# Kernel tuning notes

Measured on AMD Instinct MI355X. Metric: run time of the kernel, lower is better.

## Reference

```python
import jax, jax.numpy as jnp
import numpy as np

C = 64
DQ = C // 8  # query/key channel dim


def setup_inputs() -> dict:
    key = jax.random.key(0)
    ks = jax.random.split(key, 8)
    B, H, W = 8, 64, 64
    x = jax.random.normal(ks[0], (B, C, H, W), dtype=jnp.float32)
    # 1x1 conv weights stored as [out, in] matrices (kernel dims squeezed)
    wq = jax.random.normal(ks[1], (DQ, C), dtype=jnp.float32) * 0.05
    bq = jax.random.normal(ks[2], (DQ,), dtype=jnp.float32) * 0.05
    wk = jax.random.normal(ks[3], (DQ, C), dtype=jnp.float32) * 0.05
    bk = jax.random.normal(ks[4], (DQ,), dtype=jnp.float32) * 0.05
    wv = jax.random.normal(ks[5], (C, C), dtype=jnp.float32) * 0.05
    bv = jax.random.normal(ks[6], (C,), dtype=jnp.float32) * 0.05
    gamma = jax.random.normal(ks[7], (1,), dtype=jnp.float32)
    return {"x": x, "wq": wq, "bq": bq, "wk": wk, "bk": bk,
            "wv": wv, "bv": bv, "gamma": gamma}


def reference(x, wq, bq, wk, bk, wv, bv, gamma):
    B, Cc, H, W = x.shape
    N = H * W
    xf = x.reshape(B, Cc, N)                      # [B, C, N]
    # 1x1 convs == channel matmuls
    q = jnp.einsum('dc,bcn->bdn', wq, xf) + bq[None, :, None]   # [B, DQ, N]
    k = jnp.einsum('dc,bcn->bdn', wk, xf) + bk[None, :, None]   # [B, DQ, N]
    v = jnp.einsum('oc,bcn->bon', wv, xf) + bv[None, :, None]   # [B, C, N]
    # energy[b, m, n] = sum_d q[b, d, m] * k[b, d, n]
    energy = jnp.einsum('bdm,bdn->bmn', q, k)                   # [B, N, N]
    attention = jax.nn.softmax(energy, axis=-1)
    # out[b, c, m] = sum_n v[b, c, n] * attention[b, m, n]
    out = jnp.einsum('bcn,bmn->bcm', v, attention).reshape(B, Cc, H, W)
    return gamma[0] * out + x
```

## Files before the change

### kernel.cpp

```cpp
#include <hip/hip_runtime.h>
#include <math.h>

#define NTOK 4096
#define CCH  64
#define LOG2E 1.4426950408889634f
#define NSPLIT 4

typedef __attribute__((ext_vector_type(8)))  short bf16x8;
typedef __attribute__((ext_vector_type(4)))  float f32x4;
typedef __attribute__((ext_vector_type(16))) float f32x16;
typedef __attribute__((ext_vector_type(2)))  unsigned int uint32x2;

__device__ __forceinline__ unsigned short f2bf_rne(float f) {
    unsigned int u = __float_as_uint(f);
    u += 0x7FFFu + ((u >> 16) & 1u);
    return (unsigned short)(u >> 16);
}
__device__ __forceinline__ float bf2f(unsigned short u) {
    return __uint_as_float(((unsigned int)u) << 16);
}

__global__ __launch_bounds__(256) void proj_kernel(
    const float* __restrict__ x,
    const float* __restrict__ wq, const float* __restrict__ bq,
    const float* __restrict__ wk, const float* __restrict__ bk,
    const float* __restrict__ wv, const float* __restrict__ bv,
    unsigned short* __restrict__ qt, unsigned short* __restrict__ kt,
    unsigned short* __restrict__ vbf)
{
    __shared__ unsigned short xsb[64 * 68];
    __shared__ unsigned short wa[80 * 68];
    __shared__ unsigned short vtmp[64 * 66];
    __shared__ float bb[80];

    const int t  = threadIdx.x;
    const int b  = blockIdx.x >> 6;
    const int n0 = (blockIdx.x & 63) << 6;

    const int lane = t & 63;
    const int w    = t >> 6;
    const int l15  = lane & 15;
    const int g    = lane >> 4;

    {
        const int n  = t & 63;
        const int c0 = t >> 6;
        #pragma unroll
        for (int r = 0; r < 16; ++r) {
            const int c = c0 + 4 * r;
            xsb[n * 68 + c] = f2bf_rne(x[((size_t)(b * CCH + c)) * NTOK + n0 + n]);
        }
    }
    #pragma unroll
    for (int r = 0; r < 16; ++r) {
        const int i = t + 256 * r;
        wa[(i >> 6) * 68 + (i & 63)] = f2bf_rne(wv[i]);
    }
    {
        const int i0 = t, i1 = t + 256;
        wa[(64 + (i0 >> 6)) * 68 + (i0 & 63)] = f2bf_rne(wq[i0] * LOG2E);
        wa[(64 + (i1 >> 6)) * 68 + (i1 & 63)] = f2bf_rne(wq[i1] * LOG2E);
        wa[(72 + (i0 >> 6)) * 68 + (i0 & 63)] = f2bf_rne(wk[i0]);
        wa[(72 + (i1 >> 6)) * 68 + (i1 & 63)] = f2bf_rne(wk[i1]);
    }
    if (t < 80) {
        float bias;
        if (t < 64)      bias = bv[t];
        else if (t < 72) bias = bq[t - 64] * LOG2E;
        else             bias = bk[t - 72];
        bb[t] = bias;
    }
    __syncthreads();

    f32x4 acc[5];
    #pragma unroll
    for (int mt = 0; mt < 5; ++mt) acc[mt] = (f32x4){0.f, 0.f, 0.f, 0.f};
    #pragma unroll
    for (int kc = 0; kc < 2; ++kc) {
        const bf16x8 bx = *(const bf16x8*)&xsb[(w * 16 + l15) * 68 + kc * 32 + g * 8];
        #pragma unroll
        for (int mt = 0; mt < 5; ++mt) {
            const bf16x8 aw = *(const bf16x8*)&wa[(mt * 16 + l15) * 68 + kc * 32 + g * 8];
            acc[mt] = __builtin_amdgcn_mfma_f32_16x16x32_bf16(aw, bx, acc[mt], 0, 0, 0);
        }
    }

    const int n = w * 16 + l15;
    #pragma unroll
    for (int mt = 0; mt < 4; ++mt) {
        #pragma unroll
        for (int r = 0; r < 4; ++r) {
            const int c = mt * 16 + g * 4 + r;
            vtmp[c * 66 + 4 * l15 + w] = f2bf_rne(acc[mt][r] + bb[c]);
        }
    }
    {
        unsigned short vals[4];
        #pragma unroll
        for (int r = 0; r < 4; ++r)
            vals[r] = f2bf_rne(acc[4][r] + bb[64 + g * 4 + r]);
        const unsigned int lo = (unsigned int)vals[0] | ((unsigned int)vals[1] << 16);
        const unsigned int hi = (unsigned int)vals[2] | ((unsigned int)vals[3] << 16);
        unsigned short* dst = ((g < 2) ? qt : kt) +
                              ((size_t)(b * NTOK + n0 + n)) * 8 + (g & 1) * 4;
        *(uint32x2*)dst = (uint32x2){lo, hi};
    }
    __syncthreads();

    {
        const int c = t >> 2;
        const int q = t & 3;
        unsigned short* dst = vbf + ((size_t)(b * CCH + c)) * NTOK + n0 + q * 16;
        *(bf16x8*)dst       = *(const bf16x8*)&vtmp[c * 66 + q * 16];
        *(bf16x8*)(dst + 8) = *(const bf16x8*)&vtmp[c * 66 + q * 16 + 8];
    }
}

__global__ __launch_bounds__(256, 4) void attn_kernel(
    const unsigned short* __restrict__ qt, const unsigned short* __restrict__ kt,
    const unsigned short* __restrict__ vbf,
    unsigned short* __restrict__ opart, float* __restrict__ lpart, int B)
{
    __shared__ unsigned short qs[64 * 32];
    __shared__ unsigned short ks[64 * 40];
    __shared__ unsigned short vs[64 * 88];
    __shared__ unsigned short ps[64 * 88];

    const int t    = threadIdx.x;
    const int lane = t & 63;
    const int w    = t >> 6;
    const int p    = blockIdx.x / (B * 64);
    const int rest = blockIdx.x % (B * 64);
    const int b    = rest >> 6;
    const int m0   = (rest & 63) << 6;

    const int l15 = lane & 15;
    const int g   = lane >> 4;
    const int l31 = lane & 31;
    const int h   = lane >> 5;

    if (t < 64) {
        *(bf16x8*)&qs[t * 32] = *(const bf16x8*)&qt[((size_t)(b * NTOK + m0 + t)) * 8];
        bf16x8 z = {};
        *(bf16x8*)&qs[t * 32 + 8]  = z;
        *(bf16x8*)&qs[t * 32 + 16] = z;
        *(bf16x8*)&qs[t * 32 + 24] = z;
        *(bf16x8*)&ks[t * 40 + 8]  = z;
        *(bf16x8*)&ks[t * 40 + 16] = z;
        *(bf16x8*)&ks[t * 40 + 24] = z;
    }
    __syncthreads();

    const bf16x8 a_q = *(const bf16x8*)&qs[(w * 16 + l15) * 32 + g * 8];

    f32x16 oacc;
    #pragma unroll
    for (int i = 0; i < 16; ++i) oacc[i] = 0.f;
    float rs0 = 0.f, rs1 = 0.f, rs2 = 0.f, rs3 = 0.f;

    const int crow = ((w >> 1) * 32 + l31) * 88;
    const int mrow = ((w & 1) * 32 + l31) * 88;

    const int itEnd = p * (64 / NSPLIT) + (64 / NSPLIT);
    for (int it = p * (64 / NSPLIT); it < itEnd; ++it) {
        const int nt0 = it << 6;
        __syncthreads();

        if (t < 64)
            *(bf16x8*)&ks[t * 40] =
                *(const bf16x8*)&kt[((size_t)(b * NTOK + nt0 + t)) * 8];
        #pragma unroll
        for (int r = 0; r < 2; ++r) {
            const int i   = t + 256 * r;
            const int c   = i >> 3;
            const int seg = i & 7;
            *(bf16x8*)&vs[c * 88 + seg * 8] =
                *(const bf16x8*)&vbf[((size_t)(b * CCH + c)) * NTOK + nt0 + seg * 8];
        }
        __syncthreads();

        f32x4 s0, s1, s2, s3;
        {
            const bf16x8 bk0 = *(const bf16x8*)&ks[( 0 + l15) * 40 + g * 8];
            const bf16x8 bk1 = *(const bf16x8*)&ks[(16 + l15) * 40 + g * 8];
            const bf16x8 bk2 = *(const bf16x8*)&ks[(32 + l15) * 40 + g * 8];
            const bf16x8 bk3 = *(const bf16x8*)&ks[(48 + l15) * 40 + g * 8];
            const f32x4 z = {0.f, 0.f, 0.f, 0.f};
            s0 = __builtin_amdgcn_mfma_f32_16x16x32_bf16(a_q, bk0, z, 0, 0, 0);
            s1 = __builtin_amdgcn_mfma_f32_16x16x32_bf16(a_q, bk1, z, 0, 0, 0);
            s2 = __builtin_amdgcn_mfma_f32_16x16x32_bf16(a_q, bk2, z, 0, 0, 0);
            s3 = __builtin_amdgcn_mfma_f32_16x16x32_bf16(a_q, bk3, z, 0, 0, 0);
        }

        #pragma unroll
        for (int r = 0; r < 4; ++r) {
            const float p0 = exp2f(s0[r]);
            const float p1 = exp2f(s1[r]);
            const float p2 = exp2f(s2[r]);
            const float p3 = exp2f(s3[r]);
            const unsigned int lo = __builtin_amdgcn_perm(
                __float_as_uint(p1), __float_as_uint(p0), 0x07060302u);
            const unsigned int hi = __builtin_amdgcn_perm(
                __float_as_uint(p3), __float_as_uint(p2), 0x07060302u);
            *(uint32x2*)&ps[(w * 16 + g * 4 + r) * 88 + 4 * l15] = (uint32x2){lo, hi};
            const float ssum = (p0 + p1) + (p2 + p3);
            if      (r == 0) rs0 += ssum;
            else if (r == 1) rs1 += ssum;
            else if (r == 2) rs2 += ssum;
            else             rs3 += ssum;
        }
        __syncthreads();

        #pragma unroll
        for (int kc = 0; kc < 4; ++kc) {
            const bf16x8 a_v = *(const bf16x8*)&vs[crow + kc * 16 + h * 8];
            const bf16x8 b_p = *(const bf16x8*)&ps[mrow + kc * 16 + h * 8];
            oacc = __builtin_amdgcn_mfma_f32_32x32x16_bf16(a_v, b_p, oacc, 0, 0, 0);
        }
    }

    #pragma unroll
    for (int xm = 1; xm <= 8; xm <<= 1) {
        rs0 += __shfl_xor(rs0, xm);
        rs1 += __shfl_xor(rs1, xm);
        rs2 += __shfl_xor(rs2, xm);
        rs3 += __shfl_xor(rs3, xm);
    }
    if (l15 == 0) {
        float* lp = lpart + (size_t)(p * B + b) * NTOK + m0 + w * 16 + g * 4;
        lp[0] = rs0; lp[1] = rs1; lp[2] = rs2; lp[3] = rs3;
    }
    {
        const int mloc = (w & 1) * 32 + l31;
        #pragma unroll
        for (int reg = 0; reg < 16; ++reg) {
            const int c = (w >> 1) * 32 + (reg & 3) + 8 * (reg >> 2) + 4 * h;
            opart[((size_t)((p * B + b) * CCH + c)) * NTOK + m0 + mloc] =
                f2bf_rne(oacc[reg]);
        }
    }
}

__global__ __launch_bounds__(256) void combine_kernel(
    const unsigned short* __restrict__ opart, const float* __restrict__ lpart,
    const float* __restrict__ x, const float* __restrict__ gamma_p,
    float* __restrict__ out, int B)
{
    const float  gm      = gamma_p[0];
    const size_t nf4     = (size_t)B * CCH * NTOK / 4;
    const size_t ostride = (size_t)B * CCH * NTOK;
    for (size_t f = (size_t)blockIdx.x * 256 + threadIdx.x; f < nf4;
         f += (size_t)gridDim.x * 256) {
        const int m4 = ((int)(f & 1023)) * 4;
        const int bc = (int)(f >> 10);
        const int bi = bc >> 6;
        const size_t obase = (size_t)bc * NTOK + m4;

        float4 osum = {0.f, 0.f, 0.f, 0.f};
        float4 lsum = {0.f, 0.f, 0.f, 0.f};
        #pragma unroll
        for (int p = 0; p < NSPLIT; ++p) {
            const ushort4 o = *(const ushort4*)&opart[obase + (size_t)p * ostride];
            const float4  l = *(const float4*)&lpart[(size_t)(p * B + bi) * NTOK + m4];
            osum.x += bf2f(o.x); osum.y += bf2f(o.y);
            osum.z += bf2f(o.z); osum.w += bf2f(o.w);
            lsum.x += l.x; lsum.y += l.y; lsum.z += l.z; lsum.w += l.w;
        }
        const float4 xv = *(const float4*)&x[obase];
        float4 r;
        r.x = osum.x * gm / lsum.x + xv.x;
        r.y = osum.y * gm / lsum.y + xv.y;
        r.z = osum.z * gm / lsum.z + xv.z;
        r.w = osum.w * gm / lsum.w + xv.w;
        *(float4*)&out[obase] = r;
    }
}

extern "C" void kernel_launch(void* const* d_in, const int* in_sizes, int n_in,
                              void* d_out, int out_size, void* d_ws, size_t ws_size,
                              hipStream_t stream) {
    const float* x     = (const float*)d_in[0];
    const float* wq    = (const float*)d_in[1];
    const float* bq    = (const float*)d_in[2];
    const float* wk    = (const float*)d_in[3];
    const float* bk    = (const float*)d_in[4];
    const float* wv    = (const float*)d_in[5];
    const float* bv    = (const float*)d_in[6];
    const float* gamma = (const float*)d_in[7];
    float* out = (float*)d_out;

    int B = in_sizes[0] / (CCH * NTOK);

    unsigned short* wsp   = (unsigned short*)d_ws;
    unsigned short* qt    = wsp;
    unsigned short* kt    = qt + (size_t)B * NTOK * 8;
    unsigned short* vbf   = kt + (size_t)B * NTOK * 8;
    unsigned short* opart = vbf + (size_t)B * CCH * NTOK;
    float*          lpart = (float*)(opart + (size_t)NSPLIT * B * CCH * NTOK);

    proj_kernel<<<B * 64, 256, 0, stream>>>(x, wq, bq, wk, bk, wv, bv, qt, kt, vbf);
    attn_kernel<<<NSPLIT * B * 64, 256, 0, stream>>>(qt, kt, vbf, opart, lpart, B);
    combine_kernel<<<512, 256, 0, stream>>>(opart, lpart, x, gamma, out, B);
}
```

Baseline: 134.5 us.

## Load Q and K fragments directly from global into registers, dropping LDS staging

Measured after the change: 134.2 us. No clear change (-0.2%).

```diff
diff --git a/kernel.cpp b/kernel.cpp
--- a/kernel.cpp
+++ b/kernel.cpp
@@ -116,13 +116,11 @@
     }
 }
 
-__global__ __launch_bounds__(256, 4) void attn_kernel(
+__global__ __launch_bounds__(256, 6) void attn_kernel(
     const unsigned short* __restrict__ qt, const unsigned short* __restrict__ kt,
     const unsigned short* __restrict__ vbf,
     unsigned short* __restrict__ opart, float* __restrict__ lpart, int B)
 {
-    __shared__ unsigned short qs[64 * 32];
-    __shared__ unsigned short ks[64 * 40];
     __shared__ unsigned short vs[64 * 88];
     __shared__ unsigned short ps[64 * 88];
 
@@ -139,19 +137,9 @@
     const int l31 = lane & 31;
     const int h   = lane >> 5;
 
-    if (t < 64) {
-        *(bf16x8*)&qs[t * 32] = *(const bf16x8*)&qt[((size_t)(b * NTOK + m0 + t)) * 8];
-        bf16x8 z = {};
-        *(bf16x8*)&qs[t * 32 + 8]  = z;
-        *(bf16x8*)&qs[t * 32 + 16] = z;
-        *(bf16x8*)&qs[t * 32 + 24] = z;
-        *(bf16x8*)&ks[t * 40 + 8]  = z;
-        *(bf16x8*)&ks[t * 40 + 16] = z;
-        *(bf16x8*)&ks[t * 40 + 24] = z;
-    }
-    __syncthreads();
-
-    const bf16x8 a_q = *(const bf16x8*)&qs[(w * 16 + l15) * 32 + g * 8];
+    bf16x8 a_q = {};
+    if (g == 0)
+        a_q = *(const bf16x8*)&qt[((size_t)(b * NTOK + m0 + w * 16 + l15)) * 8];
 
     f32x16 oacc;
     #pragma unroll
@@ -166,9 +154,6 @@
         const int nt0 = it << 6;
         __syncthreads();
 
-        if (t < 64)
-            *(bf16x8*)&ks[t * 40] =
-                *(const bf16x8*)&kt[((size_t)(b * NTOK + nt0 + t)) * 8];
         #pragma unroll
         for (int r = 0; r < 2; ++r) {
             const int i   = t + 256 * r;
@@ -177,20 +162,21 @@
             *(bf16x8*)&vs[c * 88 + seg * 8] =
                 *(const bf16x8*)&vbf[((size_t)(b * CCH + c)) * NTOK + nt0 + seg * 8];
         }
-        __syncthreads();
-
-        f32x4 s0, s1, s2, s3;
-        {
-            const bf16x8 bk0 = *(const bf16x8*)&ks[( 0 + l15) * 40 + g * 8];
-            const bf16x8 bk1 = *(const bf16x8*)&ks[(16 + l15) * 40 + g * 8];
-            const bf16x8 bk2 = *(const bf16x8*)&ks[(32 + l15) * 40 + g * 8];
-            const bf16x8 bk3 = *(const bf16x8*)&ks[(48 + l15) * 40 + g * 8];
-            const f32x4 z = {0.f, 0.f, 0.f, 0.f};
-            s0 = __builtin_amdgcn_mfma_f32_16x16x32_bf16(a_q, bk0, z, 0, 0, 0);
-            s1 = __builtin_amdgcn_mfma_f32_16x16x32_bf16(a_q, bk1, z, 0, 0, 0);
-            s2 = __builtin_amdgcn_mfma_f32_16x16x32_bf16(a_q, bk2, z, 0, 0, 0);
-            s3 = __builtin_amdgcn_mfma_f32_16x16x32_bf16(a_q, bk3, z, 0, 0, 0);
-        }
+
+        bf16x8 bk0 = {}, bk1 = {}, bk2 = {}, bk3 = {};
+        if (g == 0) {
+            const unsigned short* kb = &kt[((size_t)(b * NTOK + nt0 + l15)) * 8];
+            bk0 = *(const bf16x8*)(kb);
+            bk1 = *(const bf16x8*)(kb + 16 * 8);
+            bk2 = *(const bf16x8*)(kb + 32 * 8);
+            bk3 = *(const bf16x8*)(kb + 48 * 8);
+        }
+
+        const f32x4 z = {0.f, 0.f, 0.f, 0.f};
+        f32x4 s0 = __builtin_amdgcn_mfma_f32_16x16x32_bf16(a_q, bk0, z, 0, 0, 0);
+        f32x4 s1 = __builtin_amdgcn_mfma_f32_16x16x32_bf16(a_q, bk1, z, 0, 0, 0);
+        f32x4 s2 = __builtin_amdgcn_mfma_f32_16x16x32_bf16(a_q, bk2, z, 0, 0, 0);
+        f32x4 s3 = __builtin_amdgcn_mfma_f32_16x16x32_bf16(a_q, bk3, z, 0, 0, 0);
 
         #pragma unroll
         for (int r = 0; r < 4; ++r) {
```
